# Performance work log

Hardware: AMD Instinct MI355X
Metric: run time of the kernel (lower is better)

Reference implementation:

```python
import jax, jax.numpy as jnp
import numpy as np

M = 12          # persons per frame
K = 2           # partition channels from conv1da (1024 = 2*512)
D = 512         # GCN channel dim / LSTM hidden
C_IN = 4096     # backbone feature dim
NUM_CLASSES = 8


def setup_inputs() -> dict:
    key = jax.random.key(0)
    ks = jax.random.split(key, 8)
    N, T = 16, 32
    NT = N * T
    base_out = jax.random.normal(ks[0], (NT, M, C_IN), dtype=jnp.float32)
    dist = jax.random.uniform(ks[1], (N, T, 3, K, M, M), dtype=jnp.float32)
    # conv1da: Conv1d(4096 -> 1024, k=1, bias=False) == matmul with [1024, 4096]
    w_a = jax.random.normal(ks[2], (K * D, C_IN), dtype=jnp.float32) * 0.02
    # LSTM(512, 512, 1): torch gate order i, f, g, o
    s = 1.0 / np.sqrt(D)
    w_ih = jax.random.uniform(ks[3], (4 * D, D), minval=-s, maxval=s, dtype=jnp.float32)
    w_hh = jax.random.uniform(ks[4], (4 * D, D), minval=-s, maxval=s, dtype=jnp.float32)
    b_ih = jax.random.uniform(ks[5], (4 * D,), minval=-s, maxval=s, dtype=jnp.float32)
    b_hh = jax.random.uniform(ks[6], (4 * D,), minval=-s, maxval=s, dtype=jnp.float32)
    # gclassifier: Linear(512 -> num_classes)
    w_cls = jax.random.normal(ks[7], (NUM_CLASSES, D), dtype=jnp.float32) * 0.01
    b_cls = jnp.zeros((NUM_CLASSES,), dtype=jnp.float32)
    return {"base_out": base_out, "dist": dist, "w_a": w_a,
            "w_ih": w_ih, "w_hh": w_hh, "b_ih": b_ih, "b_hh": b_hh,
            "w_cls": w_cls, "b_cls": b_cls, "n_videos": N}


def reference(base_out, dist, w_a, w_ih, w_hh, b_ih, b_hh, w_cls, b_cls, n_videos):
    NT = base_out.shape[0]
    N = n_videos
    T = NT // N
    # conv1da (1x1 conv, no bias): [NT, M, 4096] -> [NT, K*D, M] -> [NT, K, D, M]
    node1 = jnp.einsum('nmc,oc->nom', base_out, w_a).reshape(NT, K, D, M)
    # fused three-way adjacency aggregation: node1a + node1b + node1c
    A = (dist[:, :, 2] + dist[:, :, 1] + dist[:, :, 0]).reshape(NT, K, M, M)
    node = jnp.einsum('nkcv,nkvw->ncw', node1, A)  # [NT, D, M]
    node = jax.nn.relu(node)
    # AdaptiveAvgPool1d(1) over the M persons
    pooled = node.mean(axis=2)                      # [NT, D]
    seq = pooled.reshape(N, T, D)
    # torch nn.LSTM default batch_first=False: iterates over axis 0 (N), batch=T
    def step(carry, x_t):
        h, c = carry
        g = x_t @ w_ih.T + b_ih + h @ w_hh.T + b_hh  # [T, 4D]
        i, f, gg, o = jnp.split(g, 4, axis=-1)
        c = jax.nn.sigmoid(f) * c + jax.nn.sigmoid(i) * jnp.tanh(gg)
        h = jax.nn.sigmoid(o) * jnp.tanh(c)
        return (h, c), h
    h0 = jnp.zeros((T, D), dtype=seq.dtype)
    c0 = jnp.zeros((T, D), dtype=seq.dtype)
    _, hs = jax.lax.scan(step, (h0, c0), seq)       # [N, T, D]
    last = hs[:, -1, :]                              # video_feat[:, -1, :]
    return last @ w_cls.T + b_cls                    # [N, num_classes]
```

## Files before the change

kernel.cpp:

```cpp
#include <hip/hip_runtime.h>
#include <math.h>

#define MM 12
#define KK 2
#define DD 512
#define CIN 4096
#define NCLS 8
#define NV 16
#define TT 32

typedef unsigned long long u64;
typedef __attribute__((ext_vector_type(8))) __bf16 bf16x8;
typedef __attribute__((ext_vector_type(4))) float f32x4;

#define PART_F   0
#define POOLED_F 786432
#define TAGA_F   794624
#define TAGGX_F  798720
#define HGLOB_F  800768
#define GX_F     817152
#define PART_KS_STRIDE (192 * 1024)

#define MFMA_BF16(A, B, C) __builtin_amdgcn_mfma_f32_16x16x32_bf16((A), (B), (C), 0, 0, 0)
#define LOADR(p)      __hip_atomic_load((p), __ATOMIC_RELAXED, __HIP_MEMORY_SCOPE_AGENT)
#define LOADACQ(p)    __hip_atomic_load((p), __ATOMIC_ACQUIRE, __HIP_MEMORY_SCOPE_AGENT)
#define STOREREL(p, v) __hip_atomic_store((p), (v), __ATOMIC_RELEASE, __HIP_MEMORY_SCOPE_AGENT)
#define LOADS(p)      __hip_atomic_load((p), __ATOMIC_RELAXED, __HIP_MEMORY_SCOPE_SYSTEM)
#define EXCHS(p, v)   (void)__hip_atomic_exchange((p), (v), __ATOMIC_RELAXED, __HIP_MEMORY_SCOPE_SYSTEM)

static __device__ __forceinline__ u64 ld_sc0(const u64* p) {
  u64 v;
  asm volatile("global_load_dwordx2 %0, %1, off sc0\n\ts_waitcnt vmcnt(0)"
               : "=v"(v) : "v"(p) : "memory");
  return v;
}
static __device__ __forceinline__ void st_sc0(u64* p, u64 v) {
  asm volatile("global_store_dwordx2 %0, %1, off sc0" :: "v"(p), "v"(v) : "memory");
}

__global__ __launch_bounds__(256, 1) void k_gemm_pool(
    const float* __restrict__ base_out, const float* __restrict__ dist,
    const float* __restrict__ w_a,
    float* __restrict__ part, float* __restrict__ pooled,
    unsigned* __restrict__ tagA)
{
  const int wg = blockIdx.x;
  const int tid = threadIdx.x;

  __shared__ __align__(16) unsigned short Ah[16 * 40], Al[16 * 40];
  __shared__ __align__(16) unsigned short Bh[192 * 40], Bl[192 * 40];
  __shared__ float Asum_s[KK * MM * MM];

  {
    const int ks = wg >> 6, ot = wg & 63;
    const int cc0 = ks * 1024;
    const int wave = tid >> 6, lane = tid & 63;
    const int jf0 = wave * 3;

    const int sq = tid & 7;
    const int sr = tid >> 3;
    unsigned boff[6];
#pragma unroll
    for (int rep = 0; rep < 6; ++rep) {
      const int j = sr + 32 * rep;
      const int n = j / 12, m = j - n * 12;
      boff[rep] = (unsigned)(((n * TT + 31) * MM + m) * CIN + cc0 + sq * 4);
    }
    const bool aact = tid < 128;
    unsigned aoff = aact ? (unsigned)((ot * 16 + (tid >> 3)) * CIN + cc0 + sq * 4) : 0u;

    f32x4 acc0 = {0.f, 0.f, 0.f, 0.f}, acc1 = acc0, acc2 = acc0;

    float4 pa, pb[6];
    if (aact) pa = *(const float4*)&w_a[aoff];
#pragma unroll
    for (int rep = 0; rep < 6; ++rep) pb[rep] = *(const float4*)&base_out[boff[rep]];

    for (int st = 0; st < 32; ++st) {
      __syncthreads();
      if (aact) {
        const int idx = (tid >> 3) * 40 + sq * 4;
        unsigned ux = __float_as_uint(pa.x), uy = __float_as_uint(pa.y);
        unsigned uz = __float_as_uint(pa.z), uw = __float_as_uint(pa.w);
        *(uint2*)&Ah[idx] = make_uint2((ux >> 16) | (uy & 0xFFFF0000u),
                                       (uz >> 16) | (uw & 0xFFFF0000u));
        unsigned lx = __float_as_uint(pa.x - __uint_as_float(ux & 0xFFFF0000u));
        unsigned ly = __float_as_uint(pa.y - __uint_as_float(uy & 0xFFFF0000u));
        unsigned lz = __float_as_uint(pa.z - __uint_as_float(uz & 0xFFFF0000u));
        unsigned lw = __float_as_uint(pa.w - __uint_as_float(uw & 0xFFFF0000u));
        *(uint2*)&Al[idx] = make_uint2((lx >> 16) | (ly & 0xFFFF0000u),
                                       (lz >> 16) | (lw & 0xFFFF0000u));
      }
#pragma unroll
      for (int rep = 0; rep < 6; ++rep) {
        const int idx = (sr + 32 * rep) * 40 + sq * 4;
        unsigned ux = __float_as_uint(pb[rep].x), uy = __float_as_uint(pb[rep].y);
        unsigned uz = __float_as_uint(pb[rep].z), uw = __float_as_uint(pb[rep].w);
        *(uint2*)&Bh[idx] = make_uint2((ux >> 16) | (uy & 0xFFFF0000u),
                                       (uz >> 16) | (uw & 0xFFFF0000u));
        unsigned lx = __float_as_uint(pb[rep].x - __uint_as_float(ux & 0xFFFF0000u));
        unsigned ly = __float_as_uint(pb[rep].y - __uint_as_float(uy & 0xFFFF0000u));
        unsigned lz = __float_as_uint(pb[rep].z - __uint_as_float(uz & 0xFFFF0000u));
        unsigned lw = __float_as_uint(pb[rep].w - __uint_as_float(uw & 0xFFFF0000u));
        *(uint2*)&Bl[idx] = make_uint2((lx >> 16) | (ly & 0xFFFF0000u),
                                       (lz >> 16) | (lw & 0xFFFF0000u));
      }
      __syncthreads();
      if (st < 31) {
        aoff += 32;
        if (aact) pa = *(const float4*)&w_a[aoff];
#pragma unroll
        for (int rep = 0; rep < 6; ++rep) {
          boff[rep] += 32;
          pb[rep] = *(const float4*)&base_out[boff[rep]];
        }
      }
      const int koff = (lane >> 4) * 8;
      const int fra = (lane & 15) * 40 + koff;
      bf16x8 oh = *(const bf16x8*)&Ah[fra];
      bf16x8 ol = *(const bf16x8*)&Al[fra];
      {
        const int r0 = ((jf0 + 0) * 16 + (lane & 15)) * 40 + koff;
        bf16x8 jh = *(const bf16x8*)&Bh[r0], jl = *(const bf16x8*)&Bl[r0];
        acc0 = MFMA_BF16(jh, oh, acc0);
        acc0 = MFMA_BF16(jh, ol, acc0);
        acc0 = MFMA_BF16(jl, oh, acc0);
      }
      {
        const int r1 = ((jf0 + 1) * 16 + (lane & 15)) * 40 + koff;
        bf16x8 jh = *(const bf16x8*)&Bh[r1], jl = *(const bf16x8*)&Bl[r1];
        acc1 = MFMA_BF16(jh, oh, acc1);
        acc1 = MFMA_BF16(jh, ol, acc1);
        acc1 = MFMA_BF16(jl, oh, acc1);
      }
      {
        const int r2 = ((jf0 + 2) * 16 + (lane & 15)) * 40 + koff;
        bf16x8 jh = *(const bf16x8*)&Bh[r2], jl = *(const bf16x8*)&Bl[r2];
        acc2 = MFMA_BF16(jh, oh, acc2);
        acc2 = MFMA_BF16(jh, ol, acc2);
        acc2 = MFMA_BF16(jl, oh, acc2);
      }
    }
    const int o = ot * 16 + (lane & 15);
    const int jr = (lane >> 4) * 4;
#pragma unroll
    for (int r = 0; r < 4; ++r) {
      part[((size_t)ks * 192 + (jf0 + 0) * 16 + jr + r) * 1024 + o] = acc0[r];
      part[((size_t)ks * 192 + (jf0 + 1) * 16 + jr + r) * 1024 + o] = acc1[r];
      part[((size_t)ks * 192 + (jf0 + 2) * 16 + jr + r) * 1024 + o] = acc2[r];
    }
    __syncthreads();
    if (tid == 0) STOREREL(&tagA[wg * 16], 1u);
  }

  if (tid < 64) {
    bool done;
    do {
      unsigned a0 = LOADR(&tagA[(tid      ) * 16]);
      unsigned a1 = LOADR(&tagA[(tid +  64) * 16]);
      unsigned a2 = LOADR(&tagA[(tid + 128) * 16]);
      unsigned a3 = LOADR(&tagA[(tid + 192) * 16]);
      done = __all(a0 == 1u && a1 == 1u && a2 == 1u && a3 == 1u);
    } while (!done);
  }
  __syncthreads();
  (void)LOADACQ(&tagA[0]);

  {
    const int n = wg >> 4, cb = (wg & 15) * 32;
    const unsigned dbase = (unsigned)((n * TT + 31) * (3 * KK * MM * MM));
    for (int f = tid; f < KK * MM * MM; f += 256)
      Asum_s[f] = dist[dbase + f] + dist[dbase + KK * MM * MM + f]
                + dist[dbase + 2 * KK * MM * MM + f];
    __syncthreads();
    if (tid < 32) {
      const int c = cb + tid;
      float nd[KK][MM];
#pragma unroll
      for (int k = 0; k < KK; ++k)
#pragma unroll
        for (int v = 0; v < MM; ++v) {
          const size_t off = (size_t)(n * MM + v) * 1024 + k * DD + c;
          nd[k][v] = part[off] + part[off + PART_KS_STRIDE]
                   + part[off + 2 * PART_KS_STRIDE] + part[off + 3 * PART_KS_STRIDE];
        }
      float accm = 0.f;
#pragma unroll
      for (int w = 0; w < MM; ++w) {
        float sw = 0.f;
#pragma unroll
        for (int k = 0; k < KK; ++k)
#pragma unroll
          for (int v = 0; v < MM; ++v) sw += nd[k][v] * Asum_s[(k * MM + v) * MM + w];
        accm += fmaxf(sw, 0.f);
      }
      pooled[n * DD + c] = accm * (1.f / 12.f);
    }
  }
}

__global__ __launch_bounds__(1024, 1) void k_lstm(
    const float* __restrict__ pooled,
    const float* __restrict__ w_ih, const float* __restrict__ w_hh,
    const float* __restrict__ b_ih, const float* __restrict__ b_hh,
    const float* __restrict__ w_cls, const float* __restrict__ b_cls,
    unsigned* __restrict__ tagGX, float* __restrict__ gxg,
    u64* __restrict__ hg64, float* __restrict__ out)
{
  const int wg = blockIdx.x;
  const int tid = threadIdx.x;

  __shared__ __align__(16) float whh_s[64][516];
  __shared__ float gx_s[16][64];
  __shared__ __align__(16) float h_s[DD];
  __shared__ float dot_s[64];

  if ((wg & 7) != 0) {
    const int k = wg & 7;
    if (k > 4) return;
    const int m = wg >> 3;
    const int dd = m + 32 * (k - 1);
    if (tid < 256) {
      const int n = tid & 15, j = tid >> 4;
      const int gr = dd * 16 + j;
      const float4* wr = (const float4*)&w_ih[(size_t)gr * DD];
      const float4* pv = (const float4*)&pooled[(size_t)n * DD];
      float a = 0.f;
#pragma unroll 8
      for (int q = 0; q < DD / 4; ++q) {
        float4 x = wr[q], y = pv[q];
        a += x.x * y.x + x.y * y.y + x.z * y.z + x.w * y.w;
      }
      gxg[m * 1024 + n * 64 + (k - 1) * 16 + j] = a + b_ih[gr] + b_hh[gr];
    }
    __syncthreads();
    if (tid == 0) STOREREL(&tagGX[dd * 16], 1u);
    return;
  }

  const int w = wg >> 3;

  for (int f = tid; f < 64 * 128; f += 1024) {
    const int rr = f >> 7, c4 = (f & 127) * 4;
    const int grow = (rr >> 4) * DD + w * 16 + (rr & 15);
    *(float4*)&whh_s[rr][c4] = *(const float4*)&w_hh[(size_t)grow * DD + c4];
  }
  if (tid < 64) {
    bool done;
    do {
      int t0 = (int)LOADR(&tagGX[(w + 32 * (tid & 3)) * 16]);
      done = __all(t0 == 1);
    } while (!done);
  }
  __syncthreads();
  gx_s[tid >> 6][tid & 63] =
      __uint_as_float(LOADS((const unsigned*)&gxg[w * 1024 + tid]));
  __syncthreads();

  {
    float c_reg = 0.f;
    const int r = tid >> 4;
    const int lj = tid & 15;

    for (int s = 0; s < NV; ++s) {
      if (s == 0) {
        if (tid < DD) h_s[tid] = 0.f;
      } else {
        if (tid < DD) {
          const u64* p = &hg64[(size_t)(s - 1) * DD + tid];
          u64 v = ld_sc0(p);
          while ((unsigned)v != (unsigned)s) {
            v = LOADS(p);
            if ((unsigned)v == (unsigned)s) break;
            v = ld_sc0(p);
          }
          h_s[tid] = __uint_as_float((unsigned)(v >> 32));
        }
      }
      __syncthreads();

      float p = 0.f;
      const float4* wrow = (const float4*)&whh_s[r][0];
      const float4* hv4 = (const float4*)h_s;
#pragma unroll
      for (int q = 0; q < 8; ++q) {
        float4 wv = wrow[lj + 16 * q];
        float4 hv = hv4[lj + 16 * q];
        p += wv.x * hv.x + wv.y * hv.y + wv.z * hv.z + wv.w * hv.w;
      }
#pragma unroll
      for (int off = 8; off; off >>= 1) p += __shfl_down(p, off, 16);
      if (lj == 0) dot_s[r] = p;
      __syncthreads();

      if (tid < 16) {
        const float pi = gx_s[s][tid]      + dot_s[tid];
        const float pf = gx_s[s][16 + tid] + dot_s[16 + tid];
        const float pg = gx_s[s][32 + tid] + dot_s[32 + tid];
        const float po = gx_s[s][48 + tid] + dot_s[48 + tid];
        const float si = 1.f / (1.f + expf(-pi));
        const float sf = 1.f / (1.f + expf(-pf));
        const float so = 1.f / (1.f + expf(-po));
        c_reg = sf * c_reg + si * tanhf(pg);
        const float hn = so * tanhf(c_reg);
        const u64 pk = ((u64)__float_as_uint(hn) << 32) | (u64)(unsigned)(s + 1);
        u64* pp = &hg64[(size_t)s * DD + w * 16 + tid];
        st_sc0(pp, pk);
        EXCHS(pp, pk);
      }
    }
  }

  if (wg == 0) {
    float* scratch = &whh_s[0][0];
    if (tid < DD) {
      u64 vv[NV];
#pragma unroll
      for (int n = 0; n < NV; ++n) vv[n] = LOADS(&hg64[(size_t)n * DD + tid]);
#pragma unroll
      for (int n = 0; n < NV; ++n) {
        u64 v = vv[n];
        while ((unsigned)v != (unsigned)(n + 1))
          v = LOADS(&hg64[(size_t)n * DD + tid]);
        scratch[n * 516 + tid] = __uint_as_float((unsigned)(v >> 32));
      }
    }
    __syncthreads();
    if (tid < NV * NCLS) {
      const int n = tid >> 3, cl = tid & 7;
      const float4* hv = (const float4*)&scratch[n * 516];
      const float4* wv = (const float4*)(w_cls + (size_t)cl * DD);
      float a = b_cls[cl];
#pragma unroll 8
      for (int q = 0; q < DD / 4; ++q) {
        float4 x = hv[q], y = wv[q];
        a += x.x * y.x + x.y * y.y + x.z * y.z + x.w * y.w;
      }
      out[tid] = a;
    }
  }
}

extern "C" void kernel_launch(void* const* d_in, const int* in_sizes, int n_in,
                              void* d_out, int out_size, void* d_ws, size_t ws_size,
                              hipStream_t stream) {
  const float* base_out = (const float*)d_in[0];
  const float* dist     = (const float*)d_in[1];
  const float* w_a      = (const float*)d_in[2];
  const float* w_ih     = (const float*)d_in[3];
  const float* w_hh     = (const float*)d_in[4];
  const float* b_ih     = (const float*)d_in[5];
  const float* b_hh     = (const float*)d_in[6];
  const float* w_cls    = (const float*)d_in[7];
  const float* b_cls    = (const float*)d_in[8];
  float* out = (float*)d_out;

  float* ws = (float*)d_ws;
  float* part   = ws + PART_F;
  float* pooled = ws + POOLED_F;
  unsigned* tagA  = (unsigned*)(ws + TAGA_F);
  unsigned* tagGX = (unsigned*)(ws + TAGGX_F);
  u64* hg64 = (u64*)(ws + HGLOB_F);
  float* gxg = ws + GX_F;

  k_gemm_pool<<<dim3(256), 256, 0, stream>>>(base_out, dist, w_a, part, pooled, tagA);
  k_lstm<<<dim3(256), 1024, 0, stream>>>(pooled, w_ih, w_hh, b_ih, b_hh,
                                         w_cls, b_cls, tagGX, gxg, hg64, out);
}
```

Before: 282.8 us.

## Split GEMM into many single-wave blocks and move pooling into LSTM kernel

The conv GEMM now runs as 1024 one-wave workgroups, each owning a 48-row slice, instead of 256 four-wave groups that shared a B tile. The grid-wide spin barrier between the GEMM and pooling is removed. Pooling moves into the LSTM kernel as a new block role that publishes per-slice tags, and the input-projection blocks wait on those tags. This aims to spread the GEMM over more compute units and cut the barrier cost, at the price of reloading the A tile per slice and adding a new flag wait in the LSTM kernel.

New measurement: 299.0 us. 5.7% more time.

```diff
diff --git a/kernel.cpp b/kernel.cpp
--- a/kernel.cpp
+++ b/kernel.cpp
@@ -15,10 +15,10 @@
 
 #define PART_F   0
 #define POOLED_F 786432
-#define TAGA_F   794624
-#define TAGGX_F  798720
-#define HGLOB_F  800768
-#define GX_F     817152
+#define TAGP_F   794624
+#define TAGGX_F  794752
+#define HGLOB_F  796800
+#define GX_F     813184
 #define PART_KS_STRIDE (192 * 1024)
 
 #define MFMA_BF16(A, B, C) __builtin_amdgcn_mfma_f32_16x16x32_bf16((A), (B), (C), 0, 0, 0)
@@ -38,143 +38,149 @@
   asm volatile("global_store_dwordx2 %0, %1, off sc0" :: "v"(p), "v"(v) : "memory");
 }
 
-__global__ __launch_bounds__(256, 1) void k_gemm_pool(
-    const float* __restrict__ base_out, const float* __restrict__ dist,
-    const float* __restrict__ w_a,
-    float* __restrict__ part, float* __restrict__ pooled,
-    unsigned* __restrict__ tagA)
+static __device__ __forceinline__ void cvt_store(
+    unsigned short* __restrict__ hb, unsigned short* __restrict__ lb,
+    int idx, float4 v) {
+  unsigned ux = __float_as_uint(v.x), uy = __float_as_uint(v.y);
+  unsigned uz = __float_as_uint(v.z), uw = __float_as_uint(v.w);
+  *(uint2*)&hb[idx] = make_uint2((ux >> 16) | (uy & 0xFFFF0000u),
+                                 (uz >> 16) | (uw & 0xFFFF0000u));
+  unsigned lx = __float_as_uint(v.x - __uint_as_float(ux & 0xFFFF0000u));
+  unsigned ly = __float_as_uint(v.y - __uint_as_float(uy & 0xFFFF0000u));
+  unsigned lz = __float_as_uint(v.z - __uint_as_float(uz & 0xFFFF0000u));
+  unsigned lw = __float_as_uint(v.w - __uint_as_float(uw & 0xFFFF0000u));
+  *(uint2*)&lb[idx] = make_uint2((lx >> 16) | (ly & 0xFFFF0000u),
+                                 (lz >> 16) | (lw & 0xFFFF0000u));
+}
+
+__global__ __launch_bounds__(64, 1) void k_gemm(
+    const float* __restrict__ base_out, const float* __restrict__ w_a,
+    float* __restrict__ part)
+{
+  const int wg = blockIdx.x;
+  const int ks = wg & 3;
+  const int ot = (wg >> 2) & 63;
+  const int jq = (wg >> 8) & 3;
+  const int cc0 = ks * 1024;
+  const int lane = threadIdx.x;
+
+  __shared__ __align__(16) unsigned short Ah[16 * 40], Al[16 * 40];
+  __shared__ __align__(16) unsigned short Bh[48 * 40], Bl[48 * 40];
+
+  const int sq = lane & 7;
+  const int sr = lane >> 3;
+
+  unsigned boff[6];
+#pragma unroll
+  for (int rep = 0; rep < 6; ++rep) {
+    const int jl = sr + 8 * rep;
+    const int j = jq * 48 + jl;
+    const int n = j / 12, m = j - n * 12;
+    boff[rep] = (unsigned)(((n * TT + 31) * MM + m) * CIN + cc0 + sq * 4);
+  }
+  unsigned aoff[2];
+#pragma unroll
+  for (int repA = 0; repA < 2; ++repA)
+    aoff[repA] = (unsigned)((ot * 16 + sr + 8 * repA) * CIN + cc0 + sq * 4);
+
+  f32x4 acc0 = {0.f, 0.f, 0.f, 0.f}, acc1 = acc0, acc2 = acc0;
+
+  float4 pa[2], pb[6];
+#pragma unroll
+  for (int repA = 0; repA < 2; ++repA) pa[repA] = *(const float4*)&w_a[aoff[repA]];
+#pragma unroll
+  for (int rep = 0; rep < 6; ++rep) pb[rep] = *(const float4*)&base_out[boff[rep]];
+
+  for (int st = 0; st < 32; ++st) {
+#pragma unroll
+    for (int repA = 0; repA < 2; ++repA)
+      cvt_store(Ah, Al, (sr + 8 * repA) * 40 + sq * 4, pa[repA]);
+#pragma unroll
+    for (int rep = 0; rep < 6; ++rep)
+      cvt_store(Bh, Bl, (sr + 8 * rep) * 40 + sq * 4, pb[rep]);
+    if (st < 31) {
+#pragma unroll
+      for (int repA = 0; repA < 2; ++repA) {
+        aoff[repA] += 32;
+        pa[repA] = *(const float4*)&w_a[aoff[repA]];
+      }
+#pragma unroll
+      for (int rep = 0; rep < 6; ++rep) {
+        boff[rep] += 32;
+        pb[rep] = *(const float4*)&base_out[boff[rep]];
+      }
+    }
+    const int koff = (lane >> 4) * 8;
+    const int fra = (lane & 15) * 40 + koff;
+    bf16x8 oh = *(const bf16x8*)&Ah[fra];
+    bf16x8 ol = *(const bf16x8*)&Al[fra];
+    {
+      const int r0 = (0 * 16 + (lane & 15)) * 40 + koff;
+      bf16x8 jh = *(const bf16x8*)&Bh[r0], jl = *(const bf16x8*)&Bl[r0];
+      acc0 = MFMA_BF16(jh, oh, acc0);
+      acc0 = MFMA_BF16(jh, ol, acc0);
+      acc0 = MFMA_BF16(jl, oh, acc0);
+    }
+    {
+      const int r1 = (1 * 16 + (lane & 15)) * 40 + koff;
+      bf16x8 jh = *(const bf16x8*)&Bh[r1], jl = *(const bf16x8*)&Bl[r1];
+      acc1 = MFMA_BF16(jh, oh, acc1);
+      acc1 = MFMA_BF16(jh, ol, acc1);
+      acc1 = MFMA_BF16(jl, oh, acc1);
+    }
+    {
+      const int r2 = (2 * 16 + (lane & 15)) * 40 + koff;
+      bf16x8 jh = *(const bf16x8*)&Bh[r2], jl = *(const bf16x8*)&Bl[r2];
+      acc2 = MFMA_BF16(jh, oh, acc2);
+      acc2 = MFMA_BF16(jh, ol, acc2);
+      acc2 = MFMA_BF16(jl, oh, acc2);
+    }
+  }
+  const int o = ot * 16 + (lane & 15);
+  const int jr = (lane >> 4) * 4;
+#pragma unroll
+  for (int r = 0; r < 4; ++r) {
+    part[((size_t)ks * 192 + jq * 48 + 0 * 16 + jr + r) * 1024 + o] = acc0[r];
+    part[((size_t)ks * 192 + jq * 48 + 1 * 16 + jr + r) * 1024 + o] = acc1[r];
+    part[((size_t)ks * 192 + jq * 48 + 2 * 16 + jr + r) * 1024 + o] = acc2[r];
+  }
+}
+
+__global__ __launch_bounds__(1024, 1) void k_rest(
+    const float* __restrict__ dist, const float* __restrict__ part,
+    float* __restrict__ pooled,
+    const float* __restrict__ w_ih, const float* __restrict__ w_hh,
+    const float* __restrict__ b_ih, const float* __restrict__ b_hh,
+    const float* __restrict__ w_cls, const float* __restrict__ b_cls,
+    unsigned* __restrict__ tagP, unsigned* __restrict__ tagGX,
+    float* __restrict__ gxg, u64* __restrict__ hg64, float* __restrict__ out)
 {
   const int wg = blockIdx.x;
   const int tid = threadIdx.x;
 
-  __shared__ __align__(16) unsigned short Ah[16 * 40], Al[16 * 40];
-  __shared__ __align__(16) unsigned short Bh[192 * 40], Bl[192 * 40];
-  __shared__ float Asum_s[KK * MM * MM];
-
-  {
-    const int ks = wg >> 6, ot = wg & 63;
-    const int cc0 = ks * 1024;
-    const int wave = tid >> 6, lane = tid & 63;
-    const int jf0 = wave * 3;
-
-    const int sq = tid & 7;
-    const int sr = tid >> 3;
-    unsigned boff[6];
-#pragma unroll
-    for (int rep = 0; rep < 6; ++rep) {
-      const int j = sr + 32 * rep;
-      const int n = j / 12, m = j - n * 12;
-      boff[rep] = (unsigned)(((n * TT + 31) * MM + m) * CIN + cc0 + sq * 4);
-    }
-    const bool aact = tid < 128;
-    unsigned aoff = aact ? (unsigned)((ot * 16 + (tid >> 3)) * CIN + cc0 + sq * 4) : 0u;
-
-    f32x4 acc0 = {0.f, 0.f, 0.f, 0.f}, acc1 = acc0, acc2 = acc0;
-
-    float4 pa, pb[6];
-    if (aact) pa = *(const float4*)&w_a[aoff];
-#pragma unroll
-    for (int rep = 0; rep < 6; ++rep) pb[rep] = *(const float4*)&base_out[boff[rep]];
-
-    for (int st = 0; st < 32; ++st) {
-      __syncthreads();
-      if (aact) {
-        const int idx = (tid >> 3) * 40 + sq * 4;
-        unsigned ux = __float_as_uint(pa.x), uy = __float_as_uint(pa.y);
-        unsigned uz = __float_as_uint(pa.z), uw = __float_as_uint(pa.w);
-        *(uint2*)&Ah[idx] = make_uint2((ux >> 16) | (uy & 0xFFFF0000u),
-                                       (uz >> 16) | (uw & 0xFFFF0000u));
-        unsigned lx = __float_as_uint(pa.x - __uint_as_float(ux & 0xFFFF0000u));
-        unsigned ly = __float_as_uint(pa.y - __uint_as_float(uy & 0xFFFF0000u));
-        unsigned lz = __float_as_uint(pa.z - __uint_as_float(uz & 0xFFFF0000u));
-        unsigned lw = __float_as_uint(pa.w - __uint_as_float(uw & 0xFFFF0000u));
-        *(uint2*)&Al[idx] = make_uint2((lx >> 16) | (ly & 0xFFFF0000u),
-                                       (lz >> 16) | (lw & 0xFFFF0000u));
-      }
-#pragma unroll
-      for (int rep = 0; rep < 6; ++rep) {
-        const int idx = (sr + 32 * rep) * 40 + sq * 4;
-        unsigned ux = __float_as_uint(pb[rep].x), uy = __float_as_uint(pb[rep].y);
-        unsigned uz = __float_as_uint(pb[rep].z), uw = __float_as_uint(pb[rep].w);
-        *(uint2*)&Bh[idx] = make_uint2((ux >> 16) | (uy & 0xFFFF0000u),
-                                       (uz >> 16) | (uw & 0xFFFF0000u));
-        unsigned lx = __float_as_uint(pb[rep].x - __uint_as_float(ux & 0xFFFF0000u));
-        unsigned ly = __float_as_uint(pb[rep].y - __uint_as_float(uy & 0xFFFF0000u));
-        unsigned lz = __float_as_uint(pb[rep].z - __uint_as_float(uz & 0xFFFF0000u));
-        unsigned lw = __float_as_uint(pb[rep].w - __uint_as_float(uw & 0xFFFF0000u));
-        *(uint2*)&Bl[idx] = make_uint2((lx >> 16) | (ly & 0xFFFF0000u),
-                                       (lz >> 16) | (lw & 0xFFFF0000u));
-      }
-      __syncthreads();
-      if (st < 31) {
-        aoff += 32;
-        if (aact) pa = *(const float4*)&w_a[aoff];
-#pragma unroll
-        for (int rep = 0; rep < 6; ++rep) {
-          boff[rep] += 32;
-          pb[rep] = *(const float4*)&base_out[boff[rep]];
-        }
-      }
-      const int koff = (lane >> 4) * 8;
-      const int fra = (lane & 15) * 40 + koff;
-      bf16x8 oh = *(const bf16x8*)&Ah[fra];
-      bf16x8 ol = *(const bf16x8*)&Al[fra];
-      {
-        const int r0 = ((jf0 + 0) * 16 + (lane & 15)) * 40 + koff;
-        bf16x8 jh = *(const bf16x8*)&Bh[r0], jl = *(const bf16x8*)&Bl[r0];
-        acc0 = MFMA_BF16(jh, oh, acc0);
-        acc0 = MFMA_BF16(jh, ol, acc0);
-        acc0 = MFMA_BF16(jl, oh, acc0);
-      }
-      {
-        const int r1 = ((jf0 + 1) * 16 + (lane & 15)) * 40 + koff;
-        bf16x8 jh = *(const bf16x8*)&Bh[r1], jl = *(const bf16x8*)&Bl[r1];
-        acc1 = MFMA_BF16(jh, oh, acc1);
-        acc1 = MFMA_BF16(jh, ol, acc1);
-        acc1 = MFMA_BF16(jl, oh, acc1);
-      }
-      {
-        const int r2 = ((jf0 + 2) * 16 + (lane & 15)) * 40 + koff;
-        bf16x8 jh = *(const bf16x8*)&Bh[r2], jl = *(const bf16x8*)&Bl[r2];
-        acc2 = MFMA_BF16(jh, oh, acc2);
-        acc2 = MFMA_BF16(jh, ol, acc2);
-        acc2 = MFMA_BF16(jl, oh, acc2);
-      }
-    }
-    const int o = ot * 16 + (lane & 15);
-    const int jr = (lane >> 4) * 4;
-#pragma unroll
-    for (int r = 0; r < 4; ++r) {
-      part[((size_t)ks * 192 + (jf0 + 0) * 16 + jr + r) * 1024 + o] = acc0[r];
-      part[((size_t)ks * 192 + (jf0 + 1) * 16 + jr + r) * 1024 + o] = acc1[r];
-      part[((size_t)ks * 192 + (jf0 + 2) * 16 + jr + r) * 1024 + o] = acc2[r];
-    }
-    __syncthreads();
-    if (tid == 0) STOREREL(&tagA[wg * 16], 1u);
-  }
-
-  if (tid < 64) {
-    bool done;
-    do {
-      unsigned a0 = LOADR(&tagA[(tid      ) * 16]);
-      unsigned a1 = LOADR(&tagA[(tid +  64) * 16]);
-      unsigned a2 = LOADR(&tagA[(tid + 128) * 16]);
-      unsigned a3 = LOADR(&tagA[(tid + 192) * 16]);
-      done = __all(a0 == 1u && a1 == 1u && a2 == 1u && a3 == 1u);
-    } while (!done);
-  }
-  __syncthreads();
-  (void)LOADACQ(&tagA[0]);
-
-  {
-    const int n = wg >> 4, cb = (wg & 15) * 32;
-    const unsigned dbase = (unsigned)((n * TT + 31) * (3 * KK * MM * MM));
-    for (int f = tid; f < KK * MM * MM; f += 256)
-      Asum_s[f] = dist[dbase + f] + dist[dbase + KK * MM * MM + f]
-                + dist[dbase + 2 * KK * MM * MM + f];
-    __syncthreads();
-    if (tid < 32) {
-      const int c = cb + tid;
+  __shared__ __align__(16) float whh_s[64][516];
+  __shared__ float gx_s[16][64];
+  __shared__ __align__(16) float h_s[DD];
+  __shared__ float dot_s[64];
+  __shared__ float Asum_s[2][KK * MM * MM];
+
+  const int role = wg & 7;
+
+  if (role == 5) {
+    const int pq = wg >> 3;
+    if (pq >= 8) return;
+    for (int f = tid; f < 2 * KK * MM * MM; f += 1024) {
+      const int nn = f / (KK * MM * MM), ff = f - nn * (KK * MM * MM);
+      const unsigned dbase = (unsigned)(((2 * pq + nn) * TT + 31) * (3 * KK * MM * MM));
+      Asum_s[nn][ff] = dist[dbase + ff] + dist[dbase + KK * MM * MM + ff]
+                     + dist[dbase + 2 * KK * MM * MM + ff];
+    }
+    __syncthreads();
+    {
+      const int g = tid >> 5;
+      const int pwg = pq * 32 + g;
+      const int n = pwg >> 4, cb = (pwg & 15) * 32;
+      const int c = cb + (tid & 31);
       float nd[KK][MM];
 #pragma unroll
       for (int k = 0; k < KK; ++k)
@@ -191,35 +197,30 @@
 #pragma unroll
         for (int k = 0; k < KK; ++k)
 #pragma unroll
-          for (int v = 0; v < MM; ++v) sw += nd[k][v] * Asum_s[(k * MM + v) * MM + w];
+          for (int v = 0; v < MM; ++v) sw += nd[k][v] * Asum_s[n - 2 * pq][(k * MM + v) * MM + w];
         accm += fmaxf(sw, 0.f);
       }
       pooled[n * DD + c] = accm * (1.f / 12.f);
     }
-  }
-}
-
-__global__ __launch_bounds__(1024, 1) void k_lstm(
-    const float* __restrict__ pooled,
-    const float* __restrict__ w_ih, const float* __restrict__ w_hh,
-    const float* __restrict__ b_ih, const float* __restrict__ b_hh,
-    const float* __restrict__ w_cls, const float* __restrict__ b_cls,
-    unsigned* __restrict__ tagGX, float* __restrict__ gxg,
-    u64* __restrict__ hg64, float* __restrict__ out)
-{
-  const int wg = blockIdx.x;
-  const int tid = threadIdx.x;
-
-  __shared__ __align__(16) float whh_s[64][516];
-  __shared__ float gx_s[16][64];
-  __shared__ __align__(16) float h_s[DD];
-  __shared__ float dot_s[64];
-
-  if ((wg & 7) != 0) {
-    const int k = wg & 7;
+    __syncthreads();
+    if (tid == 0) STOREREL(&tagP[pq * 16], 1u);
+    return;
+  }
+
+  if (role != 0) {
+    const int k = role;
     if (k > 4) return;
     const int m = wg >> 3;
     const int dd = m + 32 * (k - 1);
+    if (tid < 64) {
+      bool done;
+      do {
+        int t0 = (int)LOADR(&tagP[(tid & 7) * 16]);
+        done = __all(t0 == 1);
+      } while (!done);
+    }
+    __syncthreads();
+    (void)LOADACQ(&tagP[0]);
     if (tid < 256) {
       const int n = tid & 15, j = tid >> 4;
       const int gr = dd * 16 + j;
@@ -358,12 +359,13 @@
   float* ws = (float*)d_ws;
   float* part   = ws + PART_F;
   float* pooled = ws + POOLED_F;
-  unsigned* tagA  = (unsigned*)(ws + TAGA_F);
+  unsigned* tagP  = (unsigned*)(ws + TAGP_F);
   unsigned* tagGX = (unsigned*)(ws + TAGGX_F);
   u64* hg64 = (u64*)(ws + HGLOB_F);
   float* gxg = ws + GX_F;
 
-  k_gemm_pool<<<dim3(256), 256, 0, stream>>>(base_out, dist, w_a, part, pooled, tagA);
-  k_lstm<<<dim3(256), 1024, 0, stream>>>(pooled, w_ih, w_hh, b_ih, b_hh,
-                                         w_cls, b_cls, tagGX, gxg, hg64, out);
-}
+  k_gemm<<<dim3(1024), 64, 0, stream>>>(base_out, w_a, part);
+  k_rest<<<dim3(256), 1024, 0, stream>>>(dist, part, pooled, w_ih, w_hh,
+                                         b_ih, b_hh, w_cls, b_cls,
+                                         tagP, tagGX, gxg, hg64, out);
+}
```
